# Kernel optimization log

Measured on AMD Instinct MI355X. Metric: run time of the kernel, lower is better.

The kernel has to match this reference:

```python
import jax, jax.numpy as jnp
import numpy as np

D, H, BS, K_TOP = 2560, 32, 32, 16
HD = D // H  # 80
B, S = 2, 1024
SCALE = HD ** -0.5


def setup_inputs() -> dict:
    key = jax.random.key(0)
    ks = jax.random.split(key, 10)
    sc = 0.02

    def lin(k, i, o):
        return (jax.random.normal(k, (i, o), jnp.float32) * sc,
                jnp.zeros((o,), jnp.float32))

    Wq, bq = lin(ks[0], D, D)
    Wk, bk = lin(ks[1], D, D)
    Wv, bv = lin(ks[2], D, D)
    Wo, bo = lin(ks[3], D, D)
    comp_W1, comp_b1 = lin(ks[4], BS * HD, 4 * HD)
    comp_W2, comp_b2 = lin(ks[5], 4 * HD, HD)
    comp_pos = jax.random.normal(ks[6], (BS, HD), jnp.float32) * sc
    gate_W1, gate_b1 = lin(ks[7], D, D // 2)
    gate_W2, gate_b2 = lin(ks[8], D // 2, 3)
    hidden_states = jax.random.normal(ks[9], (B, S, D), jnp.float32)
    return dict(hidden_states=hidden_states, Wq=Wq, bq=bq, Wk=Wk, bk=bk,
                Wv=Wv, bv=bv, Wo=Wo, bo=bo, comp_pos=comp_pos,
                comp_W1=comp_W1, comp_b1=comp_b1, comp_W2=comp_W2,
                comp_b2=comp_b2, gate_W1=gate_W1, gate_b1=gate_b1,
                gate_W2=gate_W2, gate_b2=gate_b2)


def reference(hidden_states, Wq, bq, Wk, bk, Wv, bv, Wo, bo, comp_pos,
              comp_W1, comp_b1, comp_W2, comp_b2, gate_W1, gate_b1,
              gate_W2, gate_b2):
    b, s, dm = hidden_states.shape
    blocks = s // BS

    def heads(y):  # [b,s,D] -> [b,H,s,hd]
        return y.reshape(b, s, H, HD).transpose(0, 2, 1, 3)

    q = heads(hidden_states @ Wq + bq)
    k = heads(hidden_states @ Wk + bk)
    v = heads(hidden_states @ Wv + bv)

    # --- compression branch: per-head block compression MLP (shared K/V) ---
    def compress(t):  # [b,H,s,hd] -> [b,H,blocks,hd]
        tb = t.reshape(b, H, blocks, BS, HD) + comp_pos  # pos emb per block slot
        tb = tb.reshape(b, H, blocks, BS * HD)
        h1 = jax.nn.gelu(tb @ comp_W1 + comp_b1, approximate=False)
        return h1 @ comp_W2 + comp_b2

    kc = compress(k)
    vc = compress(v)
    attn_c = jax.nn.softmax(jnp.einsum('bhsd,bhnd->bhsn', q, kc) * SCALE, axis=-1)
    out_c = jnp.einsum('bhsn,bhnd->bhsd', attn_c, vc)

    # --- dense scores, shared by selection scoring and window branch ---
    scores = jnp.einsum('bhqd,bhkd->bhqk', q, k) * SCALE  # [b,H,s,s]

    # --- selection branch: per-query top-k blocks by block-mean score ---
    block_scores = scores.reshape(b, H, s, blocks, BS).mean(-1)  # [b,H,s,blocks]
    _, top_idx = jax.lax.top_k(block_scores, K_TOP)  # [b,H,s,K]
    sel = (jnp.arange(blocks)[None, None, None, None, :] == top_idx[..., None]).any(-2)
    key_mask = jnp.repeat(sel, BS, axis=-1)  # [b,H,s,s]
    sel_scores = jnp.where(key_mask, scores, -jnp.inf)
    out_s = jnp.einsum('bhqk,bhkd->bhqd', jax.nn.softmax(sel_scores, axis=-1), v)

    # --- window branch: source's window mask is all-ones -> full attention ---
    out_w = jnp.einsum('bhqk,bhkd->bhqd', jax.nn.softmax(scores, axis=-1), v)

    # --- learned gates ---
    gh = jax.nn.gelu(hidden_states @ gate_W1 + gate_b1, approximate=False)
    gates = jax.nn.sigmoid(gh @ gate_W2 + gate_b2)  # [b,s,3]
    g = gates.transpose(2, 0, 1)[:, :, None, :, None]  # [3,b,1,s,1]
    combined = g[0] * out_c + g[1] * out_s + g[2] * out_w  # [b,H,s,hd]
    combined = combined.transpose(0, 2, 1, 3).reshape(b, s, dm)
    return combined @ Wo + bo
```

## Files before the change

kernel.cpp:

```cpp
#include <hip/hip_runtime.h>
#include <hip/hip_bf16.h>
#include <math.h>

typedef unsigned short u16;
typedef short v8s __attribute__((ext_vector_type(8)));
typedef float v4f __attribute__((ext_vector_type(4)));

#define SCALE_F 0.11180339887498949f

__device__ __forceinline__ float bf2f(u16 x) {
    unsigned int u = ((unsigned int)x) << 16;
    return __builtin_bit_cast(float, u);
}
__device__ __forceinline__ u16 f2bf(float f) {
    unsigned int u = __builtin_bit_cast(unsigned int, f);
    unsigned int r = (u + 0x7FFFu + ((u >> 16) & 1u)) >> 16;
    return (u16)r;
}
__device__ __forceinline__ float scrub(float v) {
    return (fabsf(v) < 1e30f) ? v : 0.f;
}
__device__ __forceinline__ v8s zero8() {
    union { v8s v; short s[8]; } t;
#pragma unroll
    for (int i = 0; i < 8; i++) t.s[i] = 0;
    return t.v;
}

__global__ void convX_kernel(const float* __restrict__ X, u16* __restrict__ Xb, int n)
{
    int i = (blockIdx.x * 256 + threadIdx.x) * 4;
    if (i >= n) return;
    float4 v = *(const float4*)(X + i);
    u16 o[4] = { f2bf(v.x), f2bf(v.y), f2bf(v.z), f2bf(v.w) };
    *(uint2*)(Xb + i) = *(uint2*)o;
}

__global__ __launch_bounds__(256) void convT_kernel(
    const float* __restrict__ W, u16* __restrict__ WT, int K, int N)
{
    __shared__ float t[32][33];
    int n0 = blockIdx.x * 32, k0 = blockIdx.y * 32;
    int tx = threadIdx.x & 31, ty = threadIdx.x >> 5;
    for (int i = ty; i < 32; i += 8) {
        int k = k0 + i, n = n0 + tx;
        t[i][tx] = (k < K && n < N) ? W[(size_t)k * N + n] : 0.f;
    }
    __syncthreads();
    for (int i = ty; i < 32; i += 8) {
        int n = n0 + i, k = k0 + tx;
        if (n < N && k < K) WT[(size_t)n * K + k] = f2bf(t[tx][i]);
    }
}

__global__ void xmean_kernel(const float* __restrict__ X, float* __restrict__ Xm)
{
    int c = blockIdx.x * 256 + threadIdx.x;
    if (c >= 2560) return;
    int g = blockIdx.y;
    const float* base = X + (size_t)g * 32 * 2560 + c;
    float s = 0.f;
#pragma unroll 4
    for (int j = 0; j < 32; j++) s += base[(size_t)j * 2560];
    Xm[(size_t)g * 2560 + c] = s * (1.f / 32.f);
}

__global__ __launch_bounds__(256) void gemmS_kernel(
    const float* __restrict__ A, const float* __restrict__ B,
    const float* __restrict__ bias, int M, int N, int K, float* __restrict__ outf)
{
    __shared__ __align__(16) u16 Ah[64][32], Al[64][32];
    __shared__ __align__(16) u16 Bh[64][32], Bl[64][32];
    const int tid = threadIdx.x;
    const int bm = blockIdx.x * 64, bn = blockIdx.y * 64;
    const int w = tid >> 6, lane = tid & 63;
    const int quad = lane >> 4, l = lane & 15;
    v4f acc[4];
#pragma unroll
    for (int nt = 0; nt < 4; nt++)
#pragma unroll
        for (int r = 0; r < 4; r++) acc[nt][r] = 0.f;
    const int ar = tid >> 2, ak = (tid & 3) * 8;
    const int kr = tid >> 3, nc = (tid & 7) * 8;
    for (int k0 = 0; k0 < K; k0 += 32) {
        float4 a0 = *(const float4*)(A + (size_t)(bm + ar) * K + (k0 + ak));
        float4 a1 = *(const float4*)(A + (size_t)(bm + ar) * K + (k0 + ak) + 4);
        float4 b0 = *(const float4*)(B + (size_t)(k0 + kr) * N + (bn + nc));
        float4 b1 = *(const float4*)(B + (size_t)(k0 + kr) * N + (bn + nc) + 4);
        float av[8] = {a0.x,a0.y,a0.z,a0.w,a1.x,a1.y,a1.z,a1.w};
        float bv[8] = {b0.x,b0.y,b0.z,b0.w,b1.x,b1.y,b1.z,b1.w};
        __syncthreads();
#pragma unroll
        for (int j = 0; j < 8; j++) {
            u16 h = f2bf(av[j]);
            Ah[ar][ak + j] = h; Al[ar][ak + j] = f2bf(av[j] - bf2f(h));
            u16 g = f2bf(bv[j]);
            Bh[nc + j][kr] = g; Bl[nc + j][kr] = f2bf(bv[j] - bf2f(g));
        }
        __syncthreads();
        v8s ah = *(const v8s*)(&Ah[w * 16 + l][quad * 8]);
        v8s al = *(const v8s*)(&Al[w * 16 + l][quad * 8]);
#pragma unroll
        for (int nt = 0; nt < 4; nt++) {
            v8s bh = *(const v8s*)(&Bh[nt * 16 + l][quad * 8]);
            v8s bl = *(const v8s*)(&Bl[nt * 16 + l][quad * 8]);
            acc[nt] = __builtin_amdgcn_mfma_f32_16x16x32_bf16(ah, bh, acc[nt], 0, 0, 0);
            acc[nt] = __builtin_amdgcn_mfma_f32_16x16x32_bf16(ah, bl, acc[nt], 0, 0, 0);
            acc[nt] = __builtin_amdgcn_mfma_f32_16x16x32_bf16(al, bh, acc[nt], 0, 0, 0);
        }
    }
#pragma unroll
    for (int nt = 0; nt < 4; nt++) {
        int col = bn + nt * 16 + l;
        float bvs = bias[col];
#pragma unroll
        for (int r = 0; r < 4; r++) {
            int row = bm + w * 16 + quad * 4 + r;
            outf[(size_t)row * N + col] = scrub(acc[nt][r] + bvs);
        }
    }
}

__global__ __launch_bounds__(256) void m1_kernel(
    const float* __restrict__ Wq, const float* __restrict__ km,
    u16* __restrict__ M1hT, u16* __restrict__ M1lT)
{
    __shared__ float Ws[64][81];
    __shared__ float Ks[32][80];
    int k0 = blockIdx.x * 64, h = blockIdx.y, b = blockIdx.z;
    int tid = threadIdx.x;
    for (int i = tid; i < 64 * 80; i += 256) {
        int kk = i / 80, dd = i - kk * 80;
        Ws[kk][dd] = Wq[(size_t)(k0 + kk) * 2560 + h * 80 + dd];
    }
    for (int i = tid; i < 32 * 80; i += 256) {
        int bl = i / 80, dd = i - bl * 80;
        Ks[bl][dd] = km[(size_t)((b << 5) + bl) * 2560 + h * 80 + dd];
    }
    __syncthreads();
    int kk = tid & 63, bq4 = tid >> 6;
    for (int bt = 0; bt < 8; bt++) {
        int blk = bt * 4 + bq4;
        float s = 0.f;
#pragma unroll 8
        for (int d = 0; d < 80; d++) s += Ws[kk][d] * Ks[blk][d];
        u16 hi = f2bf(s);
        size_t o = (size_t)(b * 1024 + h * 32 + blk) * 2560 + k0 + kk;
        M1hT[o] = hi;
        M1lT[o] = f2bf(s - bf2f(hi));
    }
}

__global__ void bias3_kernel(const float* __restrict__ bq, const float* __restrict__ km,
                             float* __restrict__ bias3)
{
    int i = blockIdx.x * 256 + threadIdx.x;
    if (i >= 2048) return;
    int b = i >> 10, hb = i & 1023, h = hb >> 5, blk = hb & 31;
    float s = 0.f;
    for (int d = 0; d < 80; d++) s += bq[h * 80 + d] * km[(size_t)((b << 5) + blk) * 2560 + h * 80 + d];
    bias3[i] = s;
}

__global__ __launch_bounds__(256) void gemmS2_kernel(
    const float* __restrict__ A, const u16* __restrict__ BhT, const u16* __restrict__ BlT,
    const float* __restrict__ bias, int M, int N, int K, float* __restrict__ outf)
{
    __shared__ __align__(16) u16 Ah[64][32], Al[64][32];
    __shared__ __align__(16) u16 Bh[64][32], Bl[64][32];
    const int tid = threadIdx.x;
    const int bm = blockIdx.x * 64, bn = blockIdx.y * 64;
    const int w = tid >> 6, lane = tid & 63;
    const int quad = lane >> 4, l = lane & 15;
    v4f acc[4];
#pragma unroll
    for (int nt = 0; nt < 4; nt++)
#pragma unroll
        for (int r = 0; r < 4; r++) acc[nt][r] = 0.f;
    const int ar = tid >> 2, ak = (tid & 3) * 8;
    for (int k0 = 0; k0 < K; k0 += 32) {
        float4 a0 = *(const float4*)(A + (size_t)(bm + ar) * K + (k0 + ak));
        float4 a1 = *(const float4*)(A + (size_t)(bm + ar) * K + (k0 + ak) + 4);
        float av[8] = {a0.x,a0.y,a0.z,a0.w,a1.x,a1.y,a1.z,a1.w};
        uint4 bh8 = *(const uint4*)(BhT + (size_t)(bn + ar) * K + (k0 + ak));
        uint4 bl8 = *(const uint4*)(BlT + (size_t)(bn + ar) * K + (k0 + ak));
        __syncthreads();
#pragma unroll
        for (int j = 0; j < 8; j++) {
            u16 h = f2bf(av[j]);
            Ah[ar][ak + j] = h; Al[ar][ak + j] = f2bf(av[j] - bf2f(h));
        }
        *(uint4*)(&Bh[ar][ak]) = bh8;
        *(uint4*)(&Bl[ar][ak]) = bl8;
        __syncthreads();
        v8s ah = *(const v8s*)(&Ah[w * 16 + l][quad * 8]);
        v8s al = *(const v8s*)(&Al[w * 16 + l][quad * 8]);
#pragma unroll
        for (int nt = 0; nt < 4; nt++) {
            v8s bh = *(const v8s*)(&Bh[nt * 16 + l][quad * 8]);
            v8s bl = *(const v8s*)(&Bl[nt * 16 + l][quad * 8]);
            acc[nt] = __builtin_amdgcn_mfma_f32_16x16x32_bf16(ah, bh, acc[nt], 0, 0, 0);
            acc[nt] = __builtin_amdgcn_mfma_f32_16x16x32_bf16(ah, bl, acc[nt], 0, 0, 0);
            acc[nt] = __builtin_amdgcn_mfma_f32_16x16x32_bf16(al, bh, acc[nt], 0, 0, 0);
        }
    }
#pragma unroll
    for (int nt = 0; nt < 4; nt++) {
        int col = bn + nt * 16 + l;
        float bvs = bias[col];
#pragma unroll
        for (int r = 0; r < 4; r++) {
            int row = bm + w * 16 + quad * 4 + r;
            outf[(size_t)row * N + col] = scrub(acc[nt][r] + bvs);
        }
    }
}

__global__ __launch_bounds__(256) void gemmB_kernel(
    const u16* __restrict__ A, const u16* __restrict__ Al2, const u16* __restrict__ BT,
    const float* __restrict__ bias, int M, int N, int K, int act, int ldc,
    u16* __restrict__ outb, float* __restrict__ outf, u16* __restrict__ outT)
{
    __shared__ __align__(16) u16 As[64][32];
    __shared__ __align__(16) u16 As2[64][32];
    __shared__ __align__(16) u16 Bs[64][32];
    const int tid = threadIdx.x;
    const int bm = blockIdx.x * 64, bn = blockIdx.y * 64;
    const int w = tid >> 6, lane = tid & 63;
    const int quad = lane >> 4, l = lane & 15;
    v4f acc[4];
#pragma unroll
    for (int nt = 0; nt < 4; nt++)
#pragma unroll
        for (int r = 0; r < 4; r++) acc[nt][r] = 0.f;
    const int ar = tid >> 2, ak = (tid & 3) * 8;
    for (int k0 = 0; k0 < K; k0 += 32) {
        uint4 av = *(const uint4*)(A + (size_t)(bm + ar) * K + (k0 + ak));
        uint4 av2 = make_uint4(0,0,0,0);
        if (Al2) av2 = *(const uint4*)(Al2 + (size_t)(bm + ar) * K + (k0 + ak));
        uint4 bv = make_uint4(0,0,0,0);
        if (bn + ar < N) bv = *(const uint4*)(BT + (size_t)(bn + ar) * K + (k0 + ak));
        __syncthreads();
        *(uint4*)(&As[ar][ak]) = av;
        if (Al2) *(uint4*)(&As2[ar][ak]) = av2;
        *(uint4*)(&Bs[ar][ak]) = bv;
        __syncthreads();
        v8s af = *(const v8s*)(&As[w * 16 + l][quad * 8]);
#pragma unroll
        for (int nt = 0; nt < 4; nt++) {
            v8s bf = *(const v8s*)(&Bs[nt * 16 + l][quad * 8]);
            acc[nt] = __builtin_amdgcn_mfma_f32_16x16x32_bf16(af, bf, acc[nt], 0, 0, 0);
        }
        if (Al2) {
            v8s af2 = *(const v8s*)(&As2[w * 16 + l][quad * 8]);
#pragma unroll
            for (int nt = 0; nt < 4; nt++) {
                v8s bf = *(const v8s*)(&Bs[nt * 16 + l][quad * 8]);
                acc[nt] = __builtin_amdgcn_mfma_f32_16x16x32_bf16(af2, bf, acc[nt], 0, 0, 0);
            }
        }
    }
#pragma unroll
    for (int nt = 0; nt < 4; nt++) {
        int col = bn + nt * 16 + l;
        if (col < N) {
            float bvs = bias[col];
#pragma unroll
            for (int r = 0; r < 4; r++) {
                int row = bm + w * 16 + quad * 4 + r;
                float c = acc[nt][r] + bvs;
                if (act == 1) c = 0.5f * c * (1.0f + erff(c * 0.70710678118654752f));
                c = scrub(c);
                if (outf) outf[(size_t)row * ldc + col] = c;
                if (outb) outb[(size_t)row * ldc + col] = f2bf(c);
                if (outT) {
                    int bb = row >> 10, s = row & 1023;
                    int hh = col / 80, dd = col - hh * 80;
                    outT[((size_t)((bb << 5) + hh) * 96 + dd) * 1024 + s] = f2bf(c);
                }
            }
        }
    }
}

__global__ void padv_kernel(u16* __restrict__ vt)
{
    int i = blockIdx.x * 256 + threadIdx.x;
    if (i >= 64 * 16 * 1024) return;
    int s = i & 1023, rr = (i >> 10) & 15, bh = i >> 14;
    vt[((size_t)bh * 96 + 80 + rr) * 1024 + s] = (rr == 0) ? (u16)0x3F80 : (u16)0;
}

__global__ void gatherF_kernel(const u16* __restrict__ src, const float* __restrict__ pos,
                               u16* __restrict__ F)
{
    int row = blockIdx.y;
    int col = blockIdx.x * 256 + threadIdx.x;
    if (col >= 2560) return;
    int b = row >> 10, h = (row >> 5) & 31, blk = row & 31;
    int j = col / 80, d = col - j * 80;
    float v = bf2f(src[(size_t)(b * 1024 + blk * 32 + j) * 2560 + h * 80 + d]) + pos[col];
    F[(size_t)row * 2560 + col] = f2bf(v);
}
__global__ void gatherFT_kernel(const u16* __restrict__ vt, const float* __restrict__ pos,
                                u16* __restrict__ F)
{
    int row = blockIdx.y;
    int col = blockIdx.x * 256 + threadIdx.x;
    if (col >= 2560) return;
    int b = row >> 10, h = (row >> 5) & 31, blk = row & 31;
    int j = col / 80, d = col - j * 80;
    float v = bf2f(vt[((size_t)((b << 5) + h) * 96 + d) * 1024 + blk * 32 + j]) + pos[col];
    F[(size_t)row * 2560 + col] = f2bf(v);
}

__global__ __launch_bounds__(256) void gates_kernel(
    const u16* __restrict__ gh, const float* __restrict__ W2,
    const float* __restrict__ b2, float* __restrict__ gates)
{
    int w = threadIdx.x >> 6, lane = threadIdx.x & 63;
    int token = blockIdx.x * 4 + w;
    float s0 = 0.f, s1 = 0.f, s2 = 0.f;
    for (int i = lane; i < 1280; i += 64) {
        float g = bf2f(gh[(size_t)token * 1280 + i]);
        s0 += g * W2[i * 3 + 0];
        s1 += g * W2[i * 3 + 1];
        s2 += g * W2[i * 3 + 2];
    }
#pragma unroll
    for (int m = 1; m < 64; m <<= 1) {
        s0 += __shfl_xor(s0, m);
        s1 += __shfl_xor(s1, m);
        s2 += __shfl_xor(s2, m);
    }
    if (lane == 0) {
        gates[token * 3 + 0] = scrub(1.f / (1.f + expf(-(s0 + b2[0]))));
        gates[token * 3 + 1] = scrub(1.f / (1.f + expf(-(s1 + b2[1]))));
        gates[token * 3 + 2] = scrub(1.f / (1.f + expf(-(s2 + b2[2]))));
    }
}

__global__ __launch_bounds__(64) void attn_kernel(
    const u16* __restrict__ qb, const u16* __restrict__ kbf,
    const u16* __restrict__ vt, const u16* __restrict__ kc,
    const u16* __restrict__ vc, const float* __restrict__ BSf,
    const float* __restrict__ gates, u16* __restrict__ comb, u16* __restrict__ combl)
{
    const int lane = threadIdx.x, quad = lane >> 4, l = lane & 15;
    const int qt = blockIdx.x, bh = blockIdx.y, b = bh >> 5, h = bh & 31;
    const float NEG = -1e30f;

    __shared__ float bs[16][33];
    __shared__ unsigned int selmask[16];
    __shared__ __align__(16) u16 Pw[16][40];

    {
        const float* bsrow = BSf + ((size_t)b * 1024 + qt * 16 + l) * 1024 + h * 32 + quad * 8;
#pragma unroll
        for (int i = 0; i < 8; i++) bs[l][quad * 8 + i] = bsrow[i] * SCALE_F;
    }
    __syncthreads();
    if (lane < 16) {
        unsigned int mask = 0u;
        for (int it = 0; it < 16; it++) {
            float best = NEG; int bi = -1;
            for (int n = 0; n < 32; n++) {
                if (((mask >> n) & 1u) == 0u && bs[lane][n] > best) { best = bs[lane][n]; bi = n; }
            }
            if (bi < 0) { for (int n = 0; n < 32; n++) if (((mask >> n) & 1u) == 0u) { bi = n; break; } }
            mask |= (1u << bi);
        }
        selmask[lane] = mask;
    }
    __syncthreads();
    const unsigned int selm_l = selmask[l];
    unsigned int selm[4];
#pragma unroll
    for (int r = 0; r < 4; r++) selm[r] = selmask[quad * 4 + r];
    (void)selm;

    v8s qfrag[3];
    {
        const u16* qrow = qb + (size_t)(b * 1024 + qt * 16 + l) * 2560 + h * 80;
#pragma unroll
        for (int c = 0; c < 3; c++) {
            if (c == 2 && quad >= 2) { qfrag[c] = zero8(); }
            else qfrag[c] = *(const v8s*)(qrow + c * 32 + quad * 8);
        }
    }

    v4f oc[5];
#pragma unroll
    for (int t = 0; t < 5; t++)
#pragma unroll
        for (int r = 0; r < 4; r++) oc[t][r] = 0.f;
    float l_c[4];
    {
        v4f s0, s1;
#pragma unroll
        for (int r = 0; r < 4; r++) { s0[r] = 0.f; s1[r] = 0.f; }
#pragma unroll
        for (int c = 0; c < 3; c++) {
            v8s b0, b1;
            if (c == 2 && quad >= 2) { b0 = zero8(); b1 = zero8(); }
            else {
                b0 = *(const v8s*)(kc + (size_t)(bh * 32 + l) * 80 + c * 32 + quad * 8);
                b1 = *(const v8s*)(kc + (size_t)(bh * 32 + 16 + l) * 80 + c * 32 + quad * 8);
            }
            s0 = __builtin_amdgcn_mfma_f32_16x16x32_bf16(qfrag[c], b0, s0, 0, 0, 0);
            s1 = __builtin_amdgcn_mfma_f32_16x16x32_bf16(qfrag[c], b1, s1, 0, 0, 0);
        }
#pragma unroll
        for (int r = 0; r < 4; r++) {
            float x0 = s0[r] * SCALE_F, x1 = s1[r] * SCALE_F;
            float mx = fmaxf(x0, x1);
#pragma unroll
            for (int m = 1; m < 16; m <<= 1) mx = fmaxf(mx, __shfl_xor(mx, m));
            float p0 = expf(x0 - mx), p1 = expf(x1 - mx);
            float sm = p0 + p1;
#pragma unroll
            for (int m = 1; m < 16; m <<= 1) sm += __shfl_xor(sm, m);
            l_c[r] = sm;
            Pw[quad * 4 + r][l]      = f2bf(p0);
            Pw[quad * 4 + r][l + 16] = f2bf(p1);
        }
        __syncthreads();
        v8s pa = *(const v8s*)(&Pw[l][quad * 8]);
#pragma unroll
        for (int t = 0; t < 5; t++) {
            union { v8s v; short s[8]; } vf;
#pragma unroll
            for (int j = 0; j < 8; j++)
                vf.s[j] = (short)vc[(size_t)(bh * 32 + quad * 8 + j) * 80 + t * 16 + l];
            oc[t] = __builtin_amdgcn_mfma_f32_16x16x32_bf16(pa, vf.v, oc[t], 0, 0, 0);
        }
        __syncthreads();
    }

    v4f aw[6], as_[6];
    float m_w[4];
#pragma unroll
    for (int r = 0; r < 4; r++) m_w[r] = NEG;
#pragma unroll
    for (int t = 0; t < 6; t++)
#pragma unroll
        for (int r = 0; r < 4; r++) { aw[t][r] = 0.f; as_[t][r] = 0.f; }

    const u16* vtp = vt + (size_t)bh * 96 * 1024;

    for (int kb = 0; kb < 32; kb++) {
        v4f s0, s1;
#pragma unroll
        for (int r = 0; r < 4; r++) { s0[r] = 0.f; s1[r] = 0.f; }
#pragma unroll
        for (int c = 0; c < 3; c++) {
            v8s k0f, k1f;
            if (c == 2 && quad >= 2) { k0f = zero8(); k1f = zero8(); }
            else {
                size_t base = (size_t)(b * 1024 + kb * 32) * 2560 + h * 80 + c * 32 + quad * 8;
                k0f = *(const v8s*)(kbf + base + (size_t)l * 2560);
                k1f = *(const v8s*)(kbf + base + (size_t)(16 + l) * 2560);
            }
            s0 = __builtin_amdgcn_mfma_f32_16x16x32_bf16(qfrag[c], k0f, s0, 0, 0, 0);
            s1 = __builtin_amdgcn_mfma_f32_16x16x32_bf16(qfrag[c], k1f, s1, 0, 0, 0);
        }
        float alw[4];
#pragma unroll
        for (int r = 0; r < 4; r++) {
            float x0 = s0[r] * SCALE_F, x1 = s1[r] * SCALE_F;
            float mb = fmaxf(x0, x1);
#pragma unroll
            for (int m = 1; m < 16; m <<= 1) mb = fmaxf(mb, __shfl_xor(mb, m));
            float mn = fmaxf(m_w[r], mb);
            alw[r] = expf(m_w[r] - mn);
            m_w[r] = mn;
            Pw[quad * 4 + r][l]      = f2bf(expf(x0 - mn));
            Pw[quad * 4 + r][l + 16] = f2bf(expf(x1 - mn));
        }
        __syncthreads();
        v8s pwa = *(const v8s*)(&Pw[l][quad * 8]);
        v8s psa = ((selm_l >> kb) & 1u) ? pwa : zero8();
#pragma unroll
        for (int t = 0; t < 6; t++) {
            v8s vfr = *(const v8s*)(vtp + ((size_t)(t * 16 + l)) * 1024 + kb * 32 + quad * 8);
#pragma unroll
            for (int r = 0; r < 4; r++) { aw[t][r] *= alw[r]; as_[t][r] *= alw[r]; }
            aw[t]  = __builtin_amdgcn_mfma_f32_16x16x32_bf16(pwa, vfr, aw[t], 0, 0, 0);
            as_[t] = __builtin_amdgcn_mfma_f32_16x16x32_bf16(psa, vfr, as_[t], 0, 0, 0);
        }
        __syncthreads();
    }

    float l_w[4], l_s[4];
#pragma unroll
    for (int r = 0; r < 4; r++) {
        l_w[r] = __shfl(aw[5][r], quad * 16);
        l_s[r] = __shfl(as_[5][r], quad * 16);
    }

#pragma unroll
    for (int r = 0; r < 4; r++) {
        int token = b * 1024 + qt * 16 + quad * 4 + r;
        float g0 = gates[token * 3 + 0], g1 = gates[token * 3 + 1], g2 = gates[token * 3 + 2];
        float inv_w = 1.f / fmaxf(l_w[r], 1e-30f);
        float inv_s = 1.f / fmaxf(l_s[r], 1e-30f);
        float inv_c = 1.f / fmaxf(l_c[r], 1e-30f);
#pragma unroll
        for (int t = 0; t < 5; t++) {
            float val = g0 * (oc[t][r] * inv_c) + g1 * (as_[t][r] * inv_s) + g2 * (aw[t][r] * inv_w);
            val = scrub(val);
            u16 hi = f2bf(val);
            size_t o = (size_t)token * 2560 + h * 80 + t * 16 + l;
            comb[o] = hi;
            combl[o] = f2bf(val - bf2f(hi));
        }
    }
}

extern "C" void kernel_launch(void* const* d_in, const int* in_sizes, int n_in,
                              void* d_out, int out_size, void* d_ws, size_t ws_size,
                              hipStream_t stream)
{
    (void)in_sizes; (void)n_in; (void)out_size; (void)ws_size;

    const float* X   = (const float*)d_in[0];
    const float* Wq  = (const float*)d_in[1];
    const float* bq  = (const float*)d_in[2];
    const float* Wk  = (const float*)d_in[3];
    const float* bk  = (const float*)d_in[4];
    const float* Wv  = (const float*)d_in[5];
    const float* bv  = (const float*)d_in[6];
    const float* Wo  = (const float*)d_in[7];
    const float* bo  = (const float*)d_in[8];
    const float* pos = (const float*)d_in[9];
    const float* cW1 = (const float*)d_in[10];
    const float* cb1 = (const float*)d_in[11];
    const float* cW2 = (const float*)d_in[12];
    const float* cb2 = (const float*)d_in[13];
    const float* gW1 = (const float*)d_in[14];
    const float* gb1 = (const float*)d_in[15];
    const float* gW2 = (const float*)d_in[16];
    const float* gb2 = (const float*)d_in[17];

    char* ws = (char*)d_ws;
    size_t off = 0;
    auto alloc = [&](size_t bytes) -> void* {
        void* p = ws + off;
        off += (bytes + 255) & ~(size_t)255;
        return p;
    };
    u16*   Xb     = (u16*)  alloc(2048ull * 2560 * 2);
    u16*   WqT    = (u16*)  alloc(2560ull * 2560 * 2);
    u16*   WkT    = (u16*)  alloc(2560ull * 2560 * 2);
    u16*   WvT    = (u16*)  alloc(2560ull * 2560 * 2);
    u16*   WoT    = (u16*)  alloc(2560ull * 2560 * 2);
    u16*   gW1T   = (u16*)  alloc(1280ull * 2560 * 2);
    u16*   cW1T   = (u16*)  alloc(320ull * 2560 * 2);
    u16*   cW2T   = (u16*)  alloc(96ull * 320 * 2);
    float* Xm     = (float*)alloc(64ull * 2560 * 4);
    float* kmeanS = (float*)alloc(64ull * 2560 * 4);
    u16*   M1hT   = (u16*)  alloc(2048ull * 2560 * 2);
    u16*   M1lT   = (u16*)  alloc(2048ull * 2560 * 2);
    float* bias3  = (float*)alloc(2048ull * 4);
    u16*   qbuf   = (u16*)  alloc(2048ull * 2560 * 2);
    u16*   kbf    = (u16*)  alloc(2048ull * 2560 * 2);
    u16*   vtb    = (u16*)  alloc(64ull * 96 * 1024 * 2);
    u16*   combl  = (u16*)  alloc(2048ull * 2560 * 2);
    char*  R1     = (char*) alloc(12ull * 1024 * 1024);
    u16*   gh     = (u16*)R1;
    u16*   Fb     = (u16*)R1;
    u16*   H1     = (u16*)(R1 + 10ull * 1024 * 1024);
    u16*   combb  = (u16*)R1;
    u16*   KC     = (u16*)  alloc(2048ull * 80 * 2);
    u16*   VC     = (u16*)  alloc(2048ull * 80 * 2);
    float* gatesf = (float*)alloc(2048ull * 3 * 4);
    float* BSf    = (float*)d_out;

    dim3 blk(256);
    convX_kernel<<<2048 * 2560 / 4 / 256, blk, 0, stream>>>(X, Xb, 2048 * 2560);
    convT_kernel<<<dim3(80, 80), blk, 0, stream>>>(Wq, WqT, 2560, 2560);
    convT_kernel<<<dim3(80, 80), blk, 0, stream>>>(Wk, WkT, 2560, 2560);
    convT_kernel<<<dim3(80, 80), blk, 0, stream>>>(Wv, WvT, 2560, 2560);
    convT_kernel<<<dim3(80, 80), blk, 0, stream>>>(Wo, WoT, 2560, 2560);
    convT_kernel<<<dim3(40, 80), blk, 0, stream>>>(gW1, gW1T, 2560, 1280);
    convT_kernel<<<dim3(10, 80), blk, 0, stream>>>(cW1, cW1T, 2560, 320);
    convT_kernel<<<dim3(3, 10), blk, 0, stream>>>(cW2, cW2T, 320, 80);
    xmean_kernel<<<dim3(10, 64), blk, 0, stream>>>(X, Xm);
    gemmS_kernel<<<dim3(1, 40), blk, 0, stream>>>(Xm, Wk, bk, 64, 2560, 2560, kmeanS);
    m1_kernel<<<dim3(40, 32, 2), blk, 0, stream>>>(Wq, kmeanS, M1hT, M1lT);
    bias3_kernel<<<8, blk, 0, stream>>>(bq, kmeanS, bias3);
    for (int b = 0; b < 2; b++) {
        gemmS2_kernel<<<dim3(16, 16), blk, 0, stream>>>(
            X + (size_t)b * 1024 * 2560, M1hT + (size_t)b * 1024 * 2560,
            M1lT + (size_t)b * 1024 * 2560, bias3 + b * 1024,
            1024, 1024, 2560, BSf + (size_t)b * 1024 * 1024);
    }
    gemmB_kernel<<<dim3(32, 40), blk, 0, stream>>>(Xb, nullptr, WqT, bq, 2048, 2560, 2560, 0, 2560, qbuf, nullptr, nullptr);
    gemmB_kernel<<<dim3(32, 40), blk, 0, stream>>>(Xb, nullptr, WkT, bk, 2048, 2560, 2560, 0, 2560, kbf, nullptr, nullptr);
    gemmB_kernel<<<dim3(32, 40), blk, 0, stream>>>(Xb, nullptr, WvT, bv, 2048, 2560, 2560, 0, 2560, nullptr, nullptr, vtb);
    padv_kernel<<<4096, blk, 0, stream>>>(vtb);
    gemmB_kernel<<<dim3(32, 20), blk, 0, stream>>>(Xb, nullptr, gW1T, gb1, 2048, 1280, 2560, 1, 1280, gh, nullptr, nullptr);
    gates_kernel<<<512, blk, 0, stream>>>(gh, gW2, gb2, gatesf);
    gatherF_kernel<<<dim3(10, 2048), blk, 0, stream>>>(kbf, pos, Fb);
    gemmB_kernel<<<dim3(32, 5), blk, 0, stream>>>(Fb, nullptr, cW1T, cb1, 2048, 320, 2560, 1, 320, H1, nullptr, nullptr);
    gemmB_kernel<<<dim3(32, 2), blk, 0, stream>>>(H1, nullptr, cW2T, cb2, 2048, 80, 320, 0, 80, KC, nullptr, nullptr);
    gatherFT_kernel<<<dim3(10, 2048), blk, 0, stream>>>(vtb, pos, Fb);
    gemmB_kernel<<<dim3(32, 5), blk, 0, stream>>>(Fb, nullptr, cW1T, cb1, 2048, 320, 2560, 1, 320, H1, nullptr, nullptr);
    gemmB_kernel<<<dim3(32, 2), blk, 0, stream>>>(H1, nullptr, cW2T, cb2, 2048, 80, 320, 0, 80, VC, nullptr, nullptr);
    attn_kernel<<<dim3(64, 64), 64, 0, stream>>>(qbuf, kbf, vtb, KC, VC, BSf, gatesf, combb, combl);
    gemmB_kernel<<<dim3(32, 40), blk, 0, stream>>>(combb, combl, WoT, bo, 2048, 2560, 2560, 0, 2560, nullptr, (float*)d_out, nullptr);
}
```

Baseline: 1.269 ms.

## Replace GEMMs with 128x128 async-LDS tiled kernel and restructure attention

```diff
diff --git a/kernel.cpp b/kernel.cpp
--- a/kernel.cpp
+++ b/kernel.cpp
@@ -3,6 +3,7 @@
 #include <math.h>
 
 typedef unsigned short u16;
+typedef unsigned int u32;
 typedef short v8s __attribute__((ext_vector_type(8)));
 typedef float v4f __attribute__((ext_vector_type(4)));
 
@@ -27,13 +28,27 @@
     return t.v;
 }
 
-__global__ void convX_kernel(const float* __restrict__ X, u16* __restrict__ Xb, int n)
+typedef __attribute__((address_space(3))) u32 lds_u32;
+typedef const __attribute__((address_space(1))) u32 glb_u32;
+__device__ __forceinline__ void async16(const void* g, void* l) {
+    __builtin_amdgcn_global_load_lds((glb_u32*)g, (lds_u32*)l, 16, 0, 0);
+}
+
+__global__ void convX_kernel(const float* __restrict__ X, u16* __restrict__ Xh,
+                             u16* __restrict__ Xl, int n)
 {
     int i = (blockIdx.x * 256 + threadIdx.x) * 4;
     if (i >= n) return;
     float4 v = *(const float4*)(X + i);
-    u16 o[4] = { f2bf(v.x), f2bf(v.y), f2bf(v.z), f2bf(v.w) };
-    *(uint2*)(Xb + i) = *(uint2*)o;
+    float a[4] = { v.x, v.y, v.z, v.w };
+    u16 hi[4], lo[4];
+#pragma unroll
+    for (int j = 0; j < 4; j++) {
+        hi[j] = f2bf(a[j]);
+        lo[j] = f2bf(a[j] - bf2f(hi[j]));
+    }
+    *(uint2*)(Xh + i) = *(uint2*)hi;
+    *(uint2*)(Xl + i) = *(uint2*)lo;
 }
 
 __global__ __launch_bounds__(256) void convT_kernel(
@@ -116,7 +131,7 @@
 #pragma unroll
         for (int r = 0; r < 4; r++) {
             int row = bm + w * 16 + quad * 4 + r;
-            outf[(size_t)row * N + col] = scrub(acc[nt][r] + bvs);
+            if (row < M) outf[(size_t)row * N + col] = scrub(acc[nt][r] + bvs);
         }
     }
 }
@@ -162,121 +177,81 @@
     bias3[i] = s;
 }
 
-__global__ __launch_bounds__(256) void gemmS2_kernel(
-    const float* __restrict__ A, const u16* __restrict__ BhT, const u16* __restrict__ BlT,
-    const float* __restrict__ bias, int M, int N, int K, float* __restrict__ outf)
-{
-    __shared__ __align__(16) u16 Ah[64][32], Al[64][32];
-    __shared__ __align__(16) u16 Bh[64][32], Bl[64][32];
-    const int tid = threadIdx.x;
-    const int bm = blockIdx.x * 64, bn = blockIdx.y * 64;
-    const int w = tid >> 6, lane = tid & 63;
+__global__ __launch_bounds__(256) void gemm128_kernel(
+    const u16* __restrict__ A0, const u16* __restrict__ B0,
+    const u16* __restrict__ A1, const u16* __restrict__ B1,
+    const u16* __restrict__ A2, const u16* __restrict__ B2,
+    const float* __restrict__ bias, int M, int N, int K, int act, int ldc,
+    u16* __restrict__ outb, float* __restrict__ outf,
+    u16* __restrict__ outT, u16* __restrict__ outT2)
+{
+    __shared__ __align__(16) u16 As[128][32];
+    __shared__ __align__(16) u16 Bs[128][32];
+    const int tid = threadIdx.x, w = tid >> 6, lane = tid & 63;
     const int quad = lane >> 4, l = lane & 15;
-    v4f acc[4];
-#pragma unroll
-    for (int nt = 0; nt < 4; nt++)
-#pragma unroll
-        for (int r = 0; r < 4; r++) acc[nt][r] = 0.f;
-    const int ar = tid >> 2, ak = (tid & 3) * 8;
-    for (int k0 = 0; k0 < K; k0 += 32) {
-        float4 a0 = *(const float4*)(A + (size_t)(bm + ar) * K + (k0 + ak));
-        float4 a1 = *(const float4*)(A + (size_t)(bm + ar) * K + (k0 + ak) + 4);
-        float av[8] = {a0.x,a0.y,a0.z,a0.w,a1.x,a1.y,a1.z,a1.w};
-        uint4 bh8 = *(const uint4*)(BhT + (size_t)(bn + ar) * K + (k0 + ak));
-        uint4 bl8 = *(const uint4*)(BlT + (size_t)(bn + ar) * K + (k0 + ak));
-        __syncthreads();
-#pragma unroll
-        for (int j = 0; j < 8; j++) {
-            u16 h = f2bf(av[j]);
-            Ah[ar][ak + j] = h; Al[ar][ak + j] = f2bf(av[j] - bf2f(h));
-        }
-        *(uint4*)(&Bh[ar][ak]) = bh8;
-        *(uint4*)(&Bl[ar][ak]) = bl8;
-        __syncthreads();
-        v8s ah = *(const v8s*)(&Ah[w * 16 + l][quad * 8]);
-        v8s al = *(const v8s*)(&Al[w * 16 + l][quad * 8]);
-#pragma unroll
-        for (int nt = 0; nt < 4; nt++) {
-            v8s bh = *(const v8s*)(&Bh[nt * 16 + l][quad * 8]);
-            v8s bl = *(const v8s*)(&Bl[nt * 16 + l][quad * 8]);
-            acc[nt] = __builtin_amdgcn_mfma_f32_16x16x32_bf16(ah, bh, acc[nt], 0, 0, 0);
-            acc[nt] = __builtin_amdgcn_mfma_f32_16x16x32_bf16(ah, bl, acc[nt], 0, 0, 0);
-            acc[nt] = __builtin_amdgcn_mfma_f32_16x16x32_bf16(al, bh, acc[nt], 0, 0, 0);
-        }
-    }
-#pragma unroll
-    for (int nt = 0; nt < 4; nt++) {
-        int col = bn + nt * 16 + l;
-        float bvs = bias[col];
-#pragma unroll
-        for (int r = 0; r < 4; r++) {
-            int row = bm + w * 16 + quad * 4 + r;
-            outf[(size_t)row * N + col] = scrub(acc[nt][r] + bvs);
-        }
-    }
-}
-
-__global__ __launch_bounds__(256) void gemmB_kernel(
-    const u16* __restrict__ A, const u16* __restrict__ Al2, const u16* __restrict__ BT,
-    const float* __restrict__ bias, int M, int N, int K, int act, int ldc,
-    u16* __restrict__ outb, float* __restrict__ outf, u16* __restrict__ outT)
-{
-    __shared__ __align__(16) u16 As[64][32];
-    __shared__ __align__(16) u16 As2[64][32];
-    __shared__ __align__(16) u16 Bs[64][32];
-    const int tid = threadIdx.x;
-    const int bm = blockIdx.x * 64, bn = blockIdx.y * 64;
-    const int w = tid >> 6, lane = tid & 63;
-    const int quad = lane >> 4, l = lane & 15;
-    v4f acc[4];
-#pragma unroll
-    for (int nt = 0; nt < 4; nt++)
-#pragma unroll
-        for (int r = 0; r < 4; r++) acc[nt][r] = 0.f;
-    const int ar = tid >> 2, ak = (tid & 3) * 8;
-    for (int k0 = 0; k0 < K; k0 += 32) {
-        uint4 av = *(const uint4*)(A + (size_t)(bm + ar) * K + (k0 + ak));
-        uint4 av2 = make_uint4(0,0,0,0);
-        if (Al2) av2 = *(const uint4*)(Al2 + (size_t)(bm + ar) * K + (k0 + ak));
-        uint4 bv = make_uint4(0,0,0,0);
-        if (bn + ar < N) bv = *(const uint4*)(BT + (size_t)(bn + ar) * K + (k0 + ak));
-        __syncthreads();
-        *(uint4*)(&As[ar][ak]) = av;
-        if (Al2) *(uint4*)(&As2[ar][ak]) = av2;
-        *(uint4*)(&Bs[ar][ak]) = bv;
-        __syncthreads();
-        v8s af = *(const v8s*)(&As[w * 16 + l][quad * 8]);
-#pragma unroll
-        for (int nt = 0; nt < 4; nt++) {
-            v8s bf = *(const v8s*)(&Bs[nt * 16 + l][quad * 8]);
-            acc[nt] = __builtin_amdgcn_mfma_f32_16x16x32_bf16(af, bf, acc[nt], 0, 0, 0);
-        }
-        if (Al2) {
-            v8s af2 = *(const v8s*)(&As2[w * 16 + l][quad * 8]);
-#pragma unroll
-            for (int nt = 0; nt < 4; nt++) {
-                v8s bf = *(const v8s*)(&Bs[nt * 16 + l][quad * 8]);
-                acc[nt] = __builtin_amdgcn_mfma_f32_16x16x32_bf16(af2, bf, acc[nt], 0, 0, 0);
-            }
-        }
-    }
-#pragma unroll
-    for (int nt = 0; nt < 4; nt++) {
-        int col = bn + nt * 16 + l;
+    const int bm = blockIdx.x * 128, bn = blockIdx.y * 128;
+    const int wr = (w >> 1) * 64, wc = (w & 1) * 64;
+    const int srow = lane >> 2, skoff = (lane & 3) * 8;
+
+    v4f acc[4][4];
+#pragma unroll
+    for (int i = 0; i < 4; i++)
+#pragma unroll
+        for (int j = 0; j < 4; j++)
+#pragma unroll
+            for (int r = 0; r < 4; r++) acc[i][j][r] = 0.f;
+
+    const u16* Alist[3] = { A0, A1, A2 };
+    const u16* Blist[3] = { B0, B1, B2 };
+
+    for (int seg = 0; seg < 3; seg++) {
+        const u16* Ap = Alist[seg];
+        if (!Ap) break;
+        const u16* Bp = Blist[seg];
+        for (int k0 = 0; k0 < K; k0 += 32) {
+            async16(Ap + (size_t)(bm + w * 32 + srow) * K + k0 + skoff,      &As[w * 32][0]);
+            async16(Ap + (size_t)(bm + w * 32 + 16 + srow) * K + k0 + skoff, &As[w * 32 + 16][0]);
+            async16(Bp + (size_t)(bn + w * 32 + srow) * K + k0 + skoff,      &Bs[w * 32][0]);
+            async16(Bp + (size_t)(bn + w * 32 + 16 + srow) * K + k0 + skoff, &Bs[w * 32 + 16][0]);
+            __syncthreads();
+            v8s af[4], bf[4];
+#pragma unroll
+            for (int i = 0; i < 4; i++) af[i] = *(const v8s*)(&As[wr + i * 16 + l][quad * 8]);
+#pragma unroll
+            for (int j = 0; j < 4; j++) bf[j] = *(const v8s*)(&Bs[wc + j * 16 + l][quad * 8]);
+#pragma unroll
+            for (int i = 0; i < 4; i++)
+#pragma unroll
+                for (int j = 0; j < 4; j++)
+                    acc[i][j] = __builtin_amdgcn_mfma_f32_16x16x32_bf16(af[i], bf[j], acc[i][j], 0, 0, 0);
+            __syncthreads();
+        }
+    }
+
+#pragma unroll
+    for (int j = 0; j < 4; j++) {
+        int col = bn + wc + j * 16 + l;
         if (col < N) {
             float bvs = bias[col];
 #pragma unroll
-            for (int r = 0; r < 4; r++) {
-                int row = bm + w * 16 + quad * 4 + r;
-                float c = acc[nt][r] + bvs;
-                if (act == 1) c = 0.5f * c * (1.0f + erff(c * 0.70710678118654752f));
-                c = scrub(c);
-                if (outf) outf[(size_t)row * ldc + col] = c;
-                if (outb) outb[(size_t)row * ldc + col] = f2bf(c);
-                if (outT) {
-                    int bb = row >> 10, s = row & 1023;
-                    int hh = col / 80, dd = col - hh * 80;
-                    outT[((size_t)((bb << 5) + hh) * 96 + dd) * 1024 + s] = f2bf(c);
+            for (int i = 0; i < 4; i++) {
+#pragma unroll
+                for (int r = 0; r < 4; r++) {
+                    int row = bm + wr + i * 16 + quad * 4 + r;
+                    float c = acc[i][j][r] + bvs;
+                    if (act == 1) c = 0.5f * c * (1.0f + erff(c * 0.70710678118654752f));
+                    c = scrub(c);
+                    if (outf) outf[(size_t)row * ldc + col] = c;
+                    if (outb) outb[(size_t)row * ldc + col] = f2bf(c);
+                    if (outT) {
+                        int bb = row >> 10, s = row & 1023;
+                        int hh = col / 80, dd = col - hh * 80;
+                        outT[((size_t)((bb << 5) + hh) * 96 + dd) * 1024 + s] = f2bf(c);
+                    }
+                    if (outT2) {
+                        int bh = row >> 5, blk = row & 31;
+                        outT2[((size_t)bh * 96 + col) * 32 + blk] = f2bf(c);
+                    }
                 }
             }
         }
@@ -289,6 +264,13 @@
     if (i >= 64 * 16 * 1024) return;
     int s = i & 1023, rr = (i >> 10) & 15, bh = i >> 14;
     vt[((size_t)bh * 96 + 80 + rr) * 1024 + s] = (rr == 0) ? (u16)0x3F80 : (u16)0;
+}
+__global__ void padv2_kernel(u16* __restrict__ vct)
+{
+    int i = blockIdx.x * 256 + threadIdx.x;
+    if (i >= 64 * 16 * 32) return;
+    int blk = i & 31, rr = (i >> 5) & 15, bh = i >> 9;
+    vct[((size_t)bh * 96 + 80 + rr) * 32 + blk] = (rr == 0) ? (u16)0x3F80 : (u16)0;
 }
 
 __global__ void gatherF_kernel(const u16* __restrict__ src, const float* __restrict__ pos,
@@ -340,61 +322,71 @@
     }
 }
 
-__global__ __launch_bounds__(64) void attn_kernel(
+__global__ __launch_bounds__(256, 4) void attn_kernel(
     const u16* __restrict__ qb, const u16* __restrict__ kbf,
     const u16* __restrict__ vt, const u16* __restrict__ kc,
-    const u16* __restrict__ vc, const float* __restrict__ BSf,
+    const u16* __restrict__ vct, const float* __restrict__ BSf,
     const float* __restrict__ gates, u16* __restrict__ comb, u16* __restrict__ combl)
 {
-    const int lane = threadIdx.x, quad = lane >> 4, l = lane & 15;
-    const int qt = blockIdx.x, bh = blockIdx.y, b = bh >> 5, h = bh & 31;
-    const float NEG = -1e30f;
-
-    __shared__ float bs[16][33];
-    __shared__ unsigned int selmask[16];
-    __shared__ __align__(16) u16 Pw[16][40];
-
+    const int tid = threadIdx.x, wid = tid >> 6, lane = tid & 63;
+    const int quad = lane >> 4, l = lane & 15;
+    const int qt = blockIdx.x * 4 + wid, bh = blockIdx.y, b = bh >> 5, h = bh & 31;
+
+    __shared__ float bsS[4][16][36];
+    __shared__ __align__(16) u16 PwS[4][16][40];
+    float (*bs)[36] = bsS[wid];
+    u16 (*Pw)[40] = PwS[wid];
+
+    float mine[8];
     {
-        const float* bsrow = BSf + ((size_t)b * 1024 + qt * 16 + l) * 1024 + h * 32 + quad * 8;
-#pragma unroll
-        for (int i = 0; i < 8; i++) bs[l][quad * 8 + i] = bsrow[i] * SCALE_F;
-    }
-    __syncthreads();
-    if (lane < 16) {
-        unsigned int mask = 0u;
-        for (int it = 0; it < 16; it++) {
-            float best = NEG; int bi = -1;
-            for (int n = 0; n < 32; n++) {
-                if (((mask >> n) & 1u) == 0u && bs[lane][n] > best) { best = bs[lane][n]; bi = n; }
+        const float* p = BSf + ((size_t)b << 20) + (size_t)(qt * 16 + l) * 1024 + h * 32 + quad * 8;
+        float4 v0 = *(const float4*)p, v1 = *(const float4*)(p + 4);
+        mine[0]=v0.x; mine[1]=v0.y; mine[2]=v0.z; mine[3]=v0.w;
+        mine[4]=v1.x; mine[5]=v1.y; mine[6]=v1.z; mine[7]=v1.w;
+        *(float4*)(&bs[l][quad * 8]) = v0;
+        *(float4*)(&bs[l][quad * 8 + 4]) = v1;
+    }
+    int rank[8];
+#pragma unroll
+    for (int j = 0; j < 8; j++) rank[j] = 0;
+#pragma unroll
+    for (int c4 = 0; c4 < 4; c4++) {
+        float4 o0 = *(const float4*)(&bs[l][c4 * 8]);
+        float4 o1 = *(const float4*)(&bs[l][c4 * 8 + 4]);
+        float o[8] = {o0.x,o0.y,o0.z,o0.w,o1.x,o1.y,o1.z,o1.w};
+#pragma unroll
+        for (int m = 0; m < 8; m++) {
+            int gm = c4 * 8 + m;
+#pragma unroll
+            for (int j = 0; j < 8; j++) {
+                int gj = quad * 8 + j;
+                bool better = (o[m] > mine[j]) || (o[m] == mine[j] && gm < gj);
+                rank[j] += better ? 1 : 0;
             }
-            if (bi < 0) { for (int n = 0; n < 32; n++) if (((mask >> n) & 1u) == 0u) { bi = n; break; } }
-            mask |= (1u << bi);
-        }
-        selmask[lane] = mask;
-    }
-    __syncthreads();
-    const unsigned int selm_l = selmask[l];
-    unsigned int selm[4];
-#pragma unroll
-    for (int r = 0; r < 4; r++) selm[r] = selmask[quad * 4 + r];
-    (void)selm;
+        }
+    }
+    unsigned int pm = 0;
+#pragma unroll
+    for (int j = 0; j < 8; j++) if (rank[j] < 16) pm |= 1u << (quad * 8 + j);
+    pm |= __shfl_xor(pm, 16);
+    pm |= __shfl_xor(pm, 32);
+    const unsigned int selm_l = pm;
 
     v8s qfrag[3];
     {
         const u16* qrow = qb + (size_t)(b * 1024 + qt * 16 + l) * 2560 + h * 80;
 #pragma unroll
         for (int c = 0; c < 3; c++) {
-            if (c == 2 && quad >= 2) { qfrag[c] = zero8(); }
+            if (c == 2 && quad >= 2) qfrag[c] = zero8();
             else qfrag[c] = *(const v8s*)(qrow + c * 32 + quad * 8);
         }
     }
 
-    v4f oc[5];
-#pragma unroll
-    for (int t = 0; t < 5; t++)
+    v4f oc[6];
+#pragma unroll
+    for (int t = 0; t < 6; t++)
 #pragma unroll
         for (int r = 0; r < 4; r++) oc[t][r] = 0.f;
-    float l_c[4];
     {
         v4f s0, s1;
 #pragma unroll
@@ -412,35 +404,18 @@
         }
 #pragma unroll
         for (int r = 0; r < 4; r++) {
-            float x0 = s0[r] * SCALE_F, x1 = s1[r] * SCALE_F;
-            float mx = fmaxf(x0, x1);
-#pragma unroll
-            for (int m = 1; m < 16; m <<= 1) mx = fmaxf(mx, __shfl_xor(mx, m));
-            float p0 = expf(x0 - mx), p1 = expf(x1 - mx);
-            float sm = p0 + p1;
-#pragma unroll
-            for (int m = 1; m < 16; m <<= 1) sm += __shfl_xor(sm, m);
-            l_c[r] = sm;
-            Pw[quad * 4 + r][l]      = f2bf(p0);
-            Pw[quad * 4 + r][l + 16] = f2bf(p1);
-        }
-        __syncthreads();
+            Pw[quad * 4 + r][l]      = f2bf(__expf(s0[r] * SCALE_F));
+            Pw[quad * 4 + r][l + 16] = f2bf(__expf(s1[r] * SCALE_F));
+        }
         v8s pa = *(const v8s*)(&Pw[l][quad * 8]);
 #pragma unroll
-        for (int t = 0; t < 5; t++) {
-            union { v8s v; short s[8]; } vf;
-#pragma unroll
-            for (int j = 0; j < 8; j++)
-                vf.s[j] = (short)vc[(size_t)(bh * 32 + quad * 8 + j) * 80 + t * 16 + l];
-            oc[t] = __builtin_amdgcn_mfma_f32_16x16x32_bf16(pa, vf.v, oc[t], 0, 0, 0);
-        }
-        __syncthreads();
+        for (int t = 0; t < 6; t++) {
+            v8s vfr = *(const v8s*)(vct + ((size_t)bh * 96 + t * 16 + l) * 32 + quad * 8);
+            oc[t] = __builtin_amdgcn_mfma_f32_16x16x32_bf16(pa, vfr, oc[t], 0, 0, 0);
+        }
     }
 
     v4f aw[6], as_[6];
-    float m_w[4];
-#pragma unroll
-    for (int r = 0; r < 4; r++) m_w[r] = NEG;
 #pragma unroll
     for (int t = 0; t < 6; t++)
 #pragma unroll
@@ -464,38 +439,27 @@
             s0 = __builtin_amdgcn_mfma_f32_16x16x32_bf16(qfrag[c], k0f, s0, 0, 0, 0);
             s1 = __builtin_amdgcn_mfma_f32_16x16x32_bf16(qfrag[c], k1f, s1, 0, 0, 0);
         }
-        float alw[4];
 #pragma unroll
         for (int r = 0; r < 4; r++) {
-            float x0 = s0[r] * SCALE_F, x1 = s1[r] * SCALE_F;
-            float mb = fmaxf(x0, x1);
-#pragma unroll
-            for (int m = 1; m < 16; m <<= 1) mb = fmaxf(mb, __shfl_xor(mb, m));
-            float mn = fmaxf(m_w[r], mb);
-            alw[r] = expf(m_w[r] - mn);
-            m_w[r] = mn;
-            Pw[quad * 4 + r][l]      = f2bf(expf(x0 - mn));
-            Pw[quad * 4 + r][l + 16] = f2bf(expf(x1 - mn));
-        }
-        __syncthreads();
+            Pw[quad * 4 + r][l]      = f2bf(__expf(s0[r] * SCALE_F));
+            Pw[quad * 4 + r][l + 16] = f2bf(__expf(s1[r] * SCALE_F));
+        }
         v8s pwa = *(const v8s*)(&Pw[l][quad * 8]);
         v8s psa = ((selm_l >> kb) & 1u) ? pwa : zero8();
 #pragma unroll
         for (int t = 0; t < 6; t++) {
             v8s vfr = *(const v8s*)(vtp + ((size_t)(t * 16 + l)) * 1024 + kb * 32 + quad * 8);
-#pragma unroll
-            for (int r = 0; r < 4; r++) { aw[t][r] *= alw[r]; as_[t][r] *= alw[r]; }
             aw[t]  = __builtin_amdgcn_mfma_f32_16x16x32_bf16(pwa, vfr, aw[t], 0, 0, 0);
             as_[t] = __builtin_amdgcn_mfma_f32_16x16x32_bf16(psa, vfr, as_[t], 0, 0, 0);
         }
-        __syncthreads();
-    }
-
-    float l_w[4], l_s[4];
+    }
+
+    float l_w[4], l_s[4], l_c[4];
 #pragma unroll
     for (int r = 0; r < 4; r++) {
         l_w[r] = __shfl(aw[5][r], quad * 16);
         l_s[r] = __shfl(as_[5][r], quad * 16);
+        l_c[r] = __shfl(oc[5][r], quad * 16);
     }
 
 #pragma unroll
@@ -549,35 +513,37 @@
         off += (bytes + 255) & ~(size_t)255;
         return p;
     };
-    u16*   Xb     = (u16*)  alloc(2048ull * 2560 * 2);
+    u16*   Xh     = (u16*)  alloc(2048ull * 2560 * 2);
+    u16*   Xl     = (u16*)  alloc(2048ull * 2560 * 2);
     u16*   WqT    = (u16*)  alloc(2560ull * 2560 * 2);
     u16*   WkT    = (u16*)  alloc(2560ull * 2560 * 2);
     u16*   WvT    = (u16*)  alloc(2560ull * 2560 * 2);
     u16*   WoT    = (u16*)  alloc(2560ull * 2560 * 2);
     u16*   gW1T   = (u16*)  alloc(1280ull * 2560 * 2);
-    u16*   cW1T   = (u16*)  alloc(320ull * 2560 * 2);
-    u16*   cW2T   = (u16*)  alloc(96ull * 320 * 2);
+    u16*   cW1T   = (u16*)  alloc(384ull * 2560 * 2);
+    u16*   cW2T   = (u16*)  alloc(128ull * 320 * 2);
     float* Xm     = (float*)alloc(64ull * 2560 * 4);
     float* kmeanS = (float*)alloc(64ull * 2560 * 4);
     u16*   M1hT   = (u16*)  alloc(2048ull * 2560 * 2);
     u16*   M1lT   = (u16*)  alloc(2048ull * 2560 * 2);
     float* bias3  = (float*)alloc(2048ull * 4);
-    u16*   qbuf   = (u16*)  alloc(2048ull * 2560 * 2);
     u16*   kbf    = (u16*)  alloc(2048ull * 2560 * 2);
     u16*   vtb    = (u16*)  alloc(64ull * 96 * 1024 * 2);
-    u16*   combl  = (u16*)  alloc(2048ull * 2560 * 2);
     char*  R1     = (char*) alloc(12ull * 1024 * 1024);
     u16*   gh     = (u16*)R1;
     u16*   Fb     = (u16*)R1;
     u16*   H1     = (u16*)(R1 + 10ull * 1024 * 1024);
     u16*   combb  = (u16*)R1;
     u16*   KC     = (u16*)  alloc(2048ull * 80 * 2);
-    u16*   VC     = (u16*)  alloc(2048ull * 80 * 2);
+    u16*   vct    = (u16*)  alloc(64ull * 96 * 32 * 2);
     float* gatesf = (float*)alloc(2048ull * 3 * 4);
+    alloc(64 * 1024);
+    u16*   qbuf   = M1hT;
+    u16*   combl  = M1lT;
     float* BSf    = (float*)d_out;
 
     dim3 blk(256);
-    convX_kernel<<<2048 * 2560 / 4 / 256, blk, 0, stream>>>(X, Xb, 2048 * 2560);
+    convX_kernel<<<2048 * 2560 / 4 / 256, blk, 0, stream>>>(X, Xh, Xl, 2048 * 2560);
     convT_kernel<<<dim3(80, 80), blk, 0, stream>>>(Wq, WqT, 2560, 2560);
     convT_kernel<<<dim3(80, 80), blk, 0, stream>>>(Wk, WkT, 2560, 2560);
     convT_kernel<<<dim3(80, 80), blk, 0, stream>>>(Wv, WvT, 2560, 2560);
@@ -590,23 +556,34 @@
     m1_kernel<<<dim3(40, 32, 2), blk, 0, stream>>>(Wq, kmeanS, M1hT, M1lT);
     bias3_kernel<<<8, blk, 0, stream>>>(bq, kmeanS, bias3);
     for (int b = 0; b < 2; b++) {
-        gemmS2_kernel<<<dim3(16, 16), blk, 0, stream>>>(
-            X + (size_t)b * 1024 * 2560, M1hT + (size_t)b * 1024 * 2560,
-            M1lT + (size_t)b * 1024 * 2560, bias3 + b * 1024,
-            1024, 1024, 2560, BSf + (size_t)b * 1024 * 1024);
-    }
-    gemmB_kernel<<<dim3(32, 40), blk, 0, stream>>>(Xb, nullptr, WqT, bq, 2048, 2560, 2560, 0, 2560, qbuf, nullptr, nullptr);
-    gemmB_kernel<<<dim3(32, 40), blk, 0, stream>>>(Xb, nullptr, WkT, bk, 2048, 2560, 2560, 0, 2560, kbf, nullptr, nullptr);
-    gemmB_kernel<<<dim3(32, 40), blk, 0, stream>>>(Xb, nullptr, WvT, bv, 2048, 2560, 2560, 0, 2560, nullptr, nullptr, vtb);
+        size_t ao = (size_t)b * 1024 * 2560;
+        gemm128_kernel<<<dim3(8, 8), blk, 0, stream>>>(
+            Xh + ao, M1hT + ao, Xl + ao, M1hT + ao, Xh + ao, M1lT + ao,
+            bias3 + b * 1024, 1024, 1024, 2560, 0, 1024,
+            nullptr, BSf + ((size_t)b << 20), nullptr, nullptr);
+    }
+    gemm128_kernel<<<dim3(16, 20), blk, 0, stream>>>(Xh, WqT, nullptr, nullptr, nullptr, nullptr,
+        bq, 2048, 2560, 2560, 0, 2560, qbuf, nullptr, nullptr, nullptr);
+    gemm128_kernel<<<dim3(16, 20), blk, 0, stream>>>(Xh, WkT, nullptr, nullptr, nullptr, nullptr,
+        bk, 2048, 2560, 2560, 0, 2560, kbf, nullptr, nullptr, nullptr);
+    gemm128_kernel<<<dim3(16, 20), blk, 0, stream>>>(Xh, WvT, nullptr, nullptr, nullptr, nullptr,
+        bv, 2048, 2560, 2560, 0, 2560, nullptr, nullptr, vtb, nullptr);
     padv_kernel<<<4096, blk, 0, stream>>>(vtb);
-    gemmB_kernel<<<dim3(32, 20), blk, 0, stream>>>(Xb, nullptr, gW1T, gb1, 2048, 1280, 2560, 1, 1280, gh, nullptr, nullptr);
+    gemm128_kernel<<<dim3(16, 10), blk, 0, stream>>>(Xh, gW1T, nullptr, nullptr, nullptr, nullptr,
+        gb1, 2048, 1280, 2560, 1, 1280, gh, nullptr, nullptr, nullptr);
     gates_kernel<<<512, blk, 0, stream>>>(gh, gW2, gb2, gatesf);
     gatherF_kernel<<<dim3(10, 2048), blk, 0, stream>>>(kbf, pos, Fb);
-    gemmB_kernel<<<dim3(32, 5), blk, 0, stream>>>(Fb, nullptr, cW1T, cb1, 2048, 320, 2560, 1, 320, H1, nullptr, nullptr);
-    gemmB_kernel<<<dim3(32, 2), blk, 0, stream>>>(H1, nullptr, cW2T, cb2, 2048, 80, 320, 0, 80, KC, nullptr, nullptr);
+    gemm128_kernel<<<dim3(16, 3), blk, 0, stream>>>(Fb, cW1T, nullptr, nullptr, nullptr, nullptr,
+        cb1, 2048, 320, 2560, 1, 320, H1, nullptr, nullptr, nullptr);
+    gemm128_kernel<<<dim3(16, 1), blk, 0, stream>>>(H1, cW2T, nullptr, nullptr, nullptr, nullptr,
+        cb2, 2048, 80, 320, 0, 80, KC, nullptr, nullptr, nullptr);
     gatherFT_kernel<<<dim3(10, 2048), blk, 0, stream>>>(vtb, pos, Fb);
-    gemmB_kernel<<<dim3(32, 5), blk, 0, stream>>>(Fb, nullptr, cW1T, cb1, 2048, 320, 2560, 1, 320, H1, nullptr, nullptr);
-    gemmB_kernel<<<dim3(32, 2), blk, 0, stream>>>(H1, nullptr, cW2T, cb2, 2048, 80, 320, 0, 80, VC, nullptr, nullptr);
-    attn_kernel<<<dim3(64, 64), 64, 0, stream>>>(qbuf, kbf, vtb, KC, VC, BSf, gatesf, combb, combl);
-    gemmB_kernel<<<dim3(32, 40), blk, 0, stream>>>(combb, combl, WoT, bo, 2048, 2560, 2560, 0, 2560, nullptr, (float*)d_out, nullptr);
-}
+    gemm128_kernel<<<dim3(16, 3), blk, 0, stream>>>(Fb, cW1T, nullptr, nullptr, nullptr, nullptr,
+        cb1, 2048, 320, 2560, 1, 320, H1, nullptr, nullptr, nullptr);
+    gemm128_kernel<<<dim3(16, 1), blk, 0, stream>>>(H1, cW2T, nullptr, nullptr, nullptr, nullptr,
+        cb2, 2048, 80, 320, 0, 80, nullptr, nullptr, nullptr, vct);
+    padv2_kernel<<<128, blk, 0, stream>>>(vct);
+    attn_kernel<<<dim3(16, 64), blk, 0, stream>>>(qbuf, kbf, vtb, KC, vct, BSf, gatesf, combb, combl);
+    gemm128_kernel<<<dim3(16, 20), blk, 0, stream>>>(combb, WoT, combl, WoT, nullptr, nullptr,
+        bo, 2048, 2560, 2560, 0, 2560, nullptr, (float*)d_out, nullptr, nullptr);
+}
```

Measured after the change: 1.570 ms. 23.7% more time.
